# Kernel tuning notes

Measured on AMD Instinct MI355X. Metric: run time of the kernel, lower is better.

Reference implementation:

```python
import jax, jax.numpy as jnp
import numpy as np

B, L, D = 4, 2048, 1024
N_HEADS = 16
D_KV = D // N_HEADS  # 64
TEMPERATURE = D_KV ** 0.5  # 8.0 (note: applied even though heads are never split)


def setup_inputs() -> dict:
    key = jax.random.key(0)
    ks = jax.random.split(key, 7)
    s = 1.0 / np.sqrt(D)
    return {
        "Q": jax.random.normal(ks[0], (B, L, D), jnp.float32),
        "K": jax.random.normal(ks[1], (B, L, D), jnp.float32),
        "V": jax.random.normal(ks[2], (B, L, D), jnp.float32),
        # nn.Linear weights, shape [out, in]; y = x @ W.T
        "W_Q": jax.random.normal(ks[3], (D, D), jnp.float32) * s,
        "W_K": jax.random.normal(ks[4], (D, D), jnp.float32) * s,
        "W_V": jax.random.normal(ks[5], (D, D), jnp.float32) * s,
        "W_O": jax.random.normal(ks[6], (D, D), jnp.float32) * s,
        "masked": 0,
    }


def reference(Q, K, V, W_Q, W_K, W_V, W_O, masked):
    # projections (no bias)
    q = jnp.einsum("bld,ed->ble", Q, W_Q)
    k = jnp.einsum("bld,ed->ble", K, W_K)
    v = jnp.einsum("bld,ed->ble", V, W_V)
    # NOTE: original module never splits heads; scores contract over full d_model
    scores = jnp.einsum("bqe,bke->bqk", q, k) / TEMPERATURE  # [B, L, L]
    if masked:
        # faithful (buggy) original: fill where tril is True
        tril = jnp.tril(jnp.ones((L, L), dtype=bool))
        scores = jnp.where(tril[None], -jnp.inf, scores)
    attn_weights = jax.nn.softmax(scores, axis=-1)
    # dropout(0.1) disabled (eval mode)
    x = jnp.einsum("bqk,bke->bqe", attn_weights, v)
    out = jnp.einsum("ble,de->bld", x, W_O)
    return (out, attn_weights)
```

## Files before the change

### kernel.cpp

```cpp
#include <hip/hip_runtime.h>
#include <math.h>


static constexpr int B_ = 4;
static constexpr int L_ = 2048;
static constexpr int D_ = 1024;

#define BM 128
#define BN 128
#define BKK 64

typedef _Float16 f16x8 __attribute__((ext_vector_type(8)));
typedef float    f32x4 __attribute__((ext_vector_type(4)));
typedef short    s16x8 __attribute__((ext_vector_type(8)));
typedef unsigned short u16x4 __attribute__((ext_vector_type(4)));

typedef __attribute__((address_space(1))) const unsigned int GU32;
typedef __attribute__((address_space(3))) unsigned int LU32;

__device__ __forceinline__ void gload_lds16(const void* g, void* l) {
    __builtin_amdgcn_global_load_lds((GU32*)g, (LU32*)l, 16, 0, 0);
}

__device__ __forceinline__ short f2h_bits(float x) {
    union { _Float16 h; short s; } u;
    u.h = (_Float16)x;
    return u.s;
}

__device__ __forceinline__ s16x8 cvt8h(float4 a, float4 b) {
    union { _Float16 h[8]; s16x8 s; } u;
    u.h[0] = (_Float16)a.x; u.h[1] = (_Float16)a.y;
    u.h[2] = (_Float16)a.z; u.h[3] = (_Float16)a.w;
    u.h[4] = (_Float16)b.x; u.h[5] = (_Float16)b.y;
    u.h[6] = (_Float16)b.z; u.h[7] = (_Float16)b.w;
    return u.s;
}


__device__ __forceinline__ void compute_step(
    const short* __restrict__ As, const short* __restrict__ Bs,
    int wr, int wc, int lr, int lk, f32x4 (&acc)[4][4])
{
#pragma unroll
    for (int kk = 0; kk < 2; ++kk) {
        const int slotk = kk * 4 + lk;
        f16x8 a[4], b[4];
#pragma unroll
        for (int m = 0; m < 4; ++m) {
            const int r = wr * 64 + m * 16 + lr;
            a[m] = *(const f16x8*)&As[r * 64 + ((slotk ^ (r & 7)) << 3)];
        }
#pragma unroll
        for (int n = 0; n < 4; ++n) {
            const int c = wc * 64 + n * 16 + lr;
            b[n] = *(const f16x8*)&Bs[c * 64 + ((slotk ^ (c & 7)) << 3)];
        }
#pragma unroll
        for (int m = 0; m < 4; ++m)
#pragma unroll
            for (int n = 0; n < 4; ++n)
                acc[m][n] = __builtin_amdgcn_mfma_f32_16x16x32_f16(a[m], b[n], acc[m][n], 0, 0, 0);
    }
}

template<int APPLY_SM>
__device__ __forceinline__ void epilogue_f16_bounce(
    short* __restrict__ lw, short* __restrict__ C, long N,
    int bm, int bn, int wr, int wc, int lr, int lk, int lane,
    const f32x4 (&acc)[4][4], float scale, bool msk)
{
#pragma unroll
    for (int m = 0; m < 4; ++m) {
        const int rl0 = m * 16 + lk * 4;
#pragma unroll
        for (int n = 0; n < 4; ++n) {
            const int cl = n * 16 + lr;
            const int slot = cl >> 3, cw = cl & 7;
#pragma unroll
            for (int g = 0; g < 4; ++g) {
                const int rl = rl0 + g;
                float v = acc[m][n][g];
                if constexpr (APPLY_SM) {
                    v *= scale;
                    if (msk && (bn + wc * 64 + cl) <= (bm + wr * 64 + rl)) v = -INFINITY;
                }
                lw[rl * 64 + ((slot ^ (rl & 7)) << 3) + cw] = f2h_bits(v);
            }
        }
    }
    const int l8 = lane & 7, lr8 = lane >> 3;
#pragma unroll
    for (int it = 0; it < 8; ++it) {
        const int rl = it * 8 + lr8;
        const int cl = (l8 ^ (rl & 7)) << 3;
        s16x8 d = *(const s16x8*)&lw[rl * 64 + (l8 << 3)];
        *(s16x8*)&C[(long)(bm + wr * 64 + rl) * N + bn + wc * 64 + cl] = d;
    }
}

template<int OMODE>
__global__ __launch_bounds__(256) void hgemm(
    const short* __restrict__ A16p, const short* __restrict__ Btp, void* __restrict__ Cp_,
    int M, int N, int K, long sA, long sB, long sC,
    float scale, int useMask, const int* __restrict__ mflag)
{
    __shared__ short smem[2 * BM * BKK];
    short* As = smem;
    short* Bs = smem + BM * BKK;

    const int t    = threadIdx.x;
    const int wid  = t >> 6;
    const int lane = t & 63;
    const int bz   = blockIdx.z;

    const int gx = gridDim.x, gy = gridDim.y;
    const int wg = blockIdx.y * gx + blockIdx.x;
    const int bm = (wg % gy) * BM;
    const int bn = (wg / gy) * BN;

    const short* Bt  = Btp + (long)bz * sB;
    const short* A16 = A16p + (long)bz * sA;

    const int wr = wid >> 1, wc = wid & 1;
    const int lr = lane & 15, lk = lane >> 4;
    const int srow = t >> 3, sslot = t & 7;

    f32x4 acc[4][4];
#pragma unroll
    for (int m = 0; m < 4; ++m)
#pragma unroll
        for (int n = 0; n < 4; ++n) acc[m][n] = (f32x4)0.f;

    for (int k0 = 0; k0 < K; k0 += BKK) {
        __syncthreads();
#pragma unroll
        for (int i = 0; i < 4; ++i) {
            const int rb = i * 32 + srow;
            const short* g = Bt + (long)(bn + rb) * K + k0 + ((sslot ^ (rb & 7)) << 3);
            gload_lds16(g, &Bs[i * 2048 + wid * 512]);
        }
#pragma unroll
        for (int i = 0; i < 4; ++i) {
            const int ra = i * 32 + srow;
            const short* g = A16 + (long)(bm + ra) * K + k0 + ((sslot ^ (ra & 7)) << 3);
            gload_lds16(g, &As[i * 2048 + wid * 512]);
        }
        __syncthreads();
        compute_step(As, Bs, wr, wc, lr, lk, acc);
    }

    if constexpr (OMODE == 2) {
        float* C = (float*)Cp_ + (long)bz * sC;
#pragma unroll
        for (int m = 0; m < 4; ++m) {
            const int r0 = bm + wr * 64 + m * 16 + lk * 4;
#pragma unroll
            for (int n = 0; n < 4; ++n) {
                const int c = bn + wc * 64 + n * 16 + lr;
#pragma unroll
                for (int g = 0; g < 4; ++g)
                    C[(long)(r0 + g) * N + c] = acc[m][n][g] * scale;
            }
        }
    } else {
        __syncthreads();
        short* C = (short*)Cp_ + (long)bz * sC;
        epilogue_f16_bounce<0>(smem + wid * 4096, C, N, bm, bn, wr, wc, lr, lk, lane,
                               acc, scale, false);
    }
}


__device__ __forceinline__ void stage8(
    const short* __restrict__ A16, const short* __restrict__ Bt,
    short* __restrict__ As, short* __restrict__ Bs,
    int bm, int bn, int k0, int K, int t, int wid)
{
    const int r0 = t >> 2;
    const int sl = t & 3;
#pragma unroll
    for (int i = 0; i < 2; ++i) {
        const int r = i * 128 + r0;
        const short* g = A16 + (long)(bm + r) * K + k0 + ((sl ^ ((r >> 1) & 3)) << 3);
        gload_lds16(g, As + i * 4096 + wid * 512);
    }
#pragma unroll
    for (int i = 0; i < 2; ++i) {
        const int r = i * 128 + r0;
        const short* g = Bt + (long)(bn + r) * K + k0 + ((sl ^ ((r >> 1) & 3)) << 3);
        gload_lds16(g, Bs + i * 4096 + wid * 512);
    }
}

__device__ __forceinline__ void compute32(
    const short* __restrict__ As, const short* __restrict__ Bs,
    int wr, int wc, int lr, int lk, f32x4 (&acc)[8][4])
{
    f16x8 a[8], b[4];
#pragma unroll
    for (int m = 0; m < 8; ++m) {
        const int r = wr * 128 + m * 16 + lr;
        a[m] = *(const f16x8*)&As[r * 32 + ((lk ^ ((r >> 1) & 3)) << 3)];
    }
#pragma unroll
    for (int n = 0; n < 4; ++n) {
        const int c = wc * 64 + n * 16 + lr;
        b[n] = *(const f16x8*)&Bs[c * 32 + ((lk ^ ((c >> 1) & 3)) << 3)];
    }
    __builtin_amdgcn_s_setprio(1);
#pragma unroll
    for (int m = 0; m < 8; ++m)
#pragma unroll
        for (int n = 0; n < 4; ++n)
            acc[m][n] = __builtin_amdgcn_mfma_f32_16x16x32_f16(a[m], b[n], acc[m][n], 0, 0, 0);
    __builtin_amdgcn_s_setprio(0);
}

template<int APPLY_SM>
__device__ __forceinline__ void epilogue_f16_bounce8(
    short* __restrict__ lw, short* __restrict__ C, long N,
    int rowBase, int colBase, int lr, int lk, int lane,
    const f32x4 (&acc)[8][4], float scale, bool msk)
{
#pragma unroll
    for (int h = 0; h < 2; ++h) {
#pragma unroll
        for (int mm = 0; mm < 4; ++mm) {
            const int m = h * 4 + mm;
            const int rl0 = mm * 16 + lk * 4;
#pragma unroll
            for (int n = 0; n < 4; ++n) {
                const int cl = n * 16 + lr;
                const int slot = cl >> 3, cw = cl & 7;
#pragma unroll
                for (int g = 0; g < 4; ++g) {
                    const int rl = rl0 + g;
                    float v = acc[m][n][g];
                    if constexpr (APPLY_SM) {
                        v *= scale;
                        if (msk && (colBase + cl) <= (rowBase + h * 64 + rl)) v = -INFINITY;
                    }
                    lw[rl * 64 + ((slot ^ (rl & 7)) << 3) + cw] = f2h_bits(v);
                }
            }
        }
        const int l8 = lane & 7, lr8 = lane >> 3;
#pragma unroll
        for (int it = 0; it < 8; ++it) {
            const int rl = it * 8 + lr8;
            const int cl = (l8 ^ (rl & 7)) << 3;
            s16x8 d = *(const s16x8*)&lw[rl * 64 + (l8 << 3)];
            *(s16x8*)&C[(long)(rowBase + h * 64 + rl) * N + colBase + cl] = d;
        }
    }
}

__device__ __forceinline__ void pipeline_loop(
    const short* __restrict__ A16, const short* __restrict__ Bt,
    short* __restrict__ Abuf, short* __restrict__ Bbuf,
    int bm, int bn, int K, int t, int wid,
    int wr, int wc, int lr, int lk, f32x4 (&acc)[8][4])
{
    stage8(A16, Bt, Abuf + 0 * 8192, Bbuf + 0 * 8192, bm, bn, 0,  K, t, wid);
    stage8(A16, Bt, Abuf + 1 * 8192, Bbuf + 1 * 8192, bm, bn, 32, K, t, wid);
    stage8(A16, Bt, Abuf + 2 * 8192, Bbuf + 2 * 8192, bm, bn, 64, K, t, wid);

    const int nt = K / 32;
    for (int ti = 0; ti < nt; ++ti) {
        if (ti + 2 < nt)      asm volatile("s_waitcnt vmcnt(8)" ::: "memory");
        else if (ti + 1 < nt) asm volatile("s_waitcnt vmcnt(4)" ::: "memory");
        else                  asm volatile("s_waitcnt vmcnt(0)" ::: "memory");
        __builtin_amdgcn_sched_barrier(0);
        __builtin_amdgcn_s_barrier();
        __builtin_amdgcn_sched_barrier(0);
        asm volatile("" ::: "memory");
        if (ti + 3 < nt) {
            const int nb = (ti + 3) & 3;
            stage8(A16, Bt, Abuf + nb * 8192, Bbuf + nb * 8192, bm, bn,
                   (ti + 3) * 32, K, t, wid);
        }
        const int cb = ti & 3;
        compute32(Abuf + cb * 8192, Bbuf + cb * 8192, wr, wc, lr, lk, acc);
    }
    __syncthreads();
}

__global__ __launch_bounds__(512) void hgemm8_scores(
    const short* __restrict__ qhp, const short* __restrict__ khp,
    short* __restrict__ Cp, const int* __restrict__ mflag)
{
    __shared__ short smem[65536];

    const int t    = threadIdx.x;
    const int wid  = t >> 6;
    const int lane = t & 63;
    const int bz   = blockIdx.z;
    const int K    = D_;

    const int wg = blockIdx.y * 8 + blockIdx.x;
    const int bm = (wg % 8) * 256;
    const int bn = (wg / 8) * 256;

    const short* A16 = qhp + (long)bz * L_ * D_;
    const short* Bt  = khp + (long)bz * L_ * D_;
    short* C = Cp + (long)bz * ((long)L_ * L_);

    const int wr = wid >> 2, wc = wid & 3;
    const int lr = lane & 15, lk = lane >> 4;

    f32x4 acc[8][4];
#pragma unroll
    for (int m = 0; m < 8; ++m)
#pragma unroll
        for (int n = 0; n < 4; ++n) acc[m][n] = (f32x4)0.f;

    pipeline_loop(A16, Bt, smem, smem + 32768, bm, bn, K, t, wid, wr, wc, lr, lk, acc);

    const bool msk = (mflag[0] != 0);
    epilogue_f16_bounce8<1>(smem + wid * 4096, C, L_,
                            bm + wr * 128, bn + wc * 64, lr, lk, lane,
                            acc, 0.125f, msk);
}

__global__ __launch_bounds__(512) void hgemm8_proj(
    const short* __restrict__ qf, const short* __restrict__ kf, const short* __restrict__ vf,
    const short* __restrict__ wq, const short* __restrict__ wk, const short* __restrict__ wv,
    short* __restrict__ qh, short* __restrict__ kh, short* __restrict__ vT)
{
    __shared__ short smem[65536];

    const int t    = threadIdx.x;
    const int wid  = t >> 6;
    const int lane = t & 63;
    const int bz   = blockIdx.z;
    const int K    = D_;
    const int N    = D_;

    const short* A16 = (bz == 0) ? qf : (bz == 1) ? kf : vf;
    const short* Bt  = (bz == 0) ? wq : (bz == 1) ? wk : wv;

    const int wg = blockIdx.y * 4 + blockIdx.x;
    const int bm = (wg & 31) * 256;
    const int bn = (wg >> 5) * 256;

    const int wr = wid >> 2, wc = wid & 3;
    const int lr = lane & 15, lk = lane >> 4;

    f32x4 acc[8][4];
#pragma unroll
    for (int m = 0; m < 8; ++m)
#pragma unroll
        for (int n = 0; n < 4; ++n) acc[m][n] = (f32x4)0.f;

    pipeline_loop(A16, Bt, smem, smem + 32768, bm, bn, K, t, wid, wr, wc, lr, lk, acc);

    if (bz < 2) {
        short* C = (bz == 0) ? qh : kh;
        epilogue_f16_bounce8<0>(smem + wid * 4096, C, N,
                                bm + wr * 128, bn + wc * 64, lr, lk, lane,
                                acc, 1.f, false);
    } else {
#pragma unroll
        for (int m = 0; m < 8; ++m) {
            const int rg = bm + wr * 128 + m * 16 + lk * 4;
            const long rb = (long)(rg >> 11) * ((long)N * L_) + (rg & (L_ - 1));
#pragma unroll
            for (int n = 0; n < 4; ++n) {
                const int c = bn + wc * 64 + n * 16 + lr;
                u16x4 v;
#pragma unroll
                for (int g = 0; g < 4; ++g) v[g] = (unsigned short)f2h_bits(acc[m][n][g]);
                *(u16x4*)&vT[rb + (long)c * L_] = v;
            }
        }
    }
}


__global__ __launch_bounds__(256) void cvt_w4_k(
    const float* __restrict__ W_Q, const float* __restrict__ W_K,
    const float* __restrict__ W_V, const float* __restrict__ W_O,
    short* __restrict__ dst)
{
    const int w = blockIdx.y;
    const float* src = (w == 0) ? W_Q : (w == 1) ? W_K : (w == 2) ? W_V : W_O;
    short* out = dst + (size_t)w * D_ * D_;
    const int i = blockIdx.x * 256 + threadIdx.x;
    float4 a = ((const float4*)src)[2 * i];
    float4 b = ((const float4*)src)[2 * i + 1];
    *(s16x8*)&out[i * 8] = cvt8h(a, b);
}

__global__ __launch_bounds__(256) void cvt_qkv_k(
    const float* __restrict__ Q, const float* __restrict__ K,
    const float* __restrict__ V, short* __restrict__ dst)
{
    const int w = blockIdx.y;
    const float* src = (w == 0) ? Q : (w == 1) ? K : V;
    short* out = dst + (size_t)w * B_ * L_ * D_;
    const int i = blockIdx.x * 256 + threadIdx.x;
    float4 a = ((const float4*)src)[2 * i];
    float4 b = ((const float4*)src)[2 * i + 1];
    *(s16x8*)&out[i * 8] = cvt8h(a, b);
}

__global__ __launch_bounds__(256) void softmax_rows_k(
    short* __restrict__ S16, float* __restrict__ Sout)
{
    const long row = blockIdx.x;
    short* p16 = S16 + row * (long)L_;
    float* pf  = Sout + row * (long)L_;
    const int tid = threadIdx.x;

    union { s16x8 v; _Float16 h[8]; } u;
    u.v = ((const s16x8*)p16)[tid];
    float f[8];
#pragma unroll
    for (int j = 0; j < 8; ++j) f[j] = (float)u.h[j];

    float m = f[0];
#pragma unroll
    for (int j = 1; j < 8; ++j) m = fmaxf(m, f[j]);
#pragma unroll
    for (int o = 32; o > 0; o >>= 1) m = fmaxf(m, __shfl_xor(m, o, 64));

    __shared__ float wmax[4], wsum[4];
    if ((tid & 63) == 0) wmax[tid >> 6] = m;
    __syncthreads();
    m = fmaxf(fmaxf(wmax[0], wmax[1]), fmaxf(wmax[2], wmax[3]));

    float s = 0.f;
#pragma unroll
    for (int j = 0; j < 8; ++j) { f[j] = expf(f[j] - m); s += f[j]; }
#pragma unroll
    for (int o = 32; o > 0; o >>= 1) s += __shfl_xor(s, o, 64);
    if ((tid & 63) == 0) wsum[tid >> 6] = s;
    __syncthreads();
    s = wsum[0] + wsum[1] + wsum[2] + wsum[3];

    const float inv = 1.f / s;
#pragma unroll
    for (int j = 0; j < 8; ++j) f[j] = f[j] * inv;

    float4 a, b;
    a.x = f[0]; a.y = f[1]; a.z = f[2]; a.w = f[3];
    b.x = f[4]; b.y = f[5]; b.z = f[6]; b.w = f[7];
    ((float4*)pf)[2 * tid]     = a;
    ((float4*)pf)[2 * tid + 1] = b;
    ((s16x8*)p16)[tid] = cvt8h(a, b);
}

extern "C" void kernel_launch(void* const* d_in, const int* in_sizes, int n_in,
                              void* d_out, int out_size, void* d_ws, size_t ws_size,
                              hipStream_t stream) {
    const float* Q   = (const float*)d_in[0];
    const float* K   = (const float*)d_in[1];
    const float* V   = (const float*)d_in[2];
    const float* W_Q = (const float*)d_in[3];
    const float* W_K = (const float*)d_in[4];
    const float* W_V = (const float*)d_in[5];
    const float* W_O = (const float*)d_in[6];
    const int* masked = (const int*)d_in[7];

    float* out  = (float*)d_out;
    float* attn = out + (size_t)B_ * L_ * D_;

    short* wq = (short*)d_ws;
    short* wk = wq + (size_t)D_ * D_;
    short* wv = wk + (size_t)D_ * D_;
    short* wo = wv + (size_t)D_ * D_;
    short* qh = wo + (size_t)D_ * D_;
    short* kh = qh + (size_t)B_ * L_ * D_;
    short* vT = kh + (size_t)B_ * L_ * D_;
    short* attn16 = vT + (size_t)B_ * L_ * D_;
    short* xh = qh;

    short* qf = (short*)attn;
    short* kf = qf + (size_t)B_ * L_ * D_;
    short* vf = kf + (size_t)B_ * L_ * D_;

    const long SLD = (long)L_ * D_;
    const long SLL = (long)L_ * L_;

    cvt_w4_k<<<dim3(D_ * D_ / 8 / 256, 4), 256, 0, stream>>>(W_Q, W_K, W_V, W_O, wq);
    cvt_qkv_k<<<dim3(B_ * L_ * D_ / 8 / 256, 3), 256, 0, stream>>>(Q, K, V, qf);

    hgemm8_proj<<<dim3(4, 32, 3), 512, 0, stream>>>(
        qf, kf, vf, wq, wk, wv, qh, kh, vT);

    hgemm8_scores<<<dim3(8, 8, B_), 512, 0, stream>>>(qh, kh, attn16, masked);

    softmax_rows_k<<<dim3(B_ * L_), 256, 0, stream>>>(attn16, attn);

    dim3 gav(D_ / BN, L_ / BM, B_);
    hgemm<0><<<gav, 256, 0, stream>>>(attn16, vT, xh, L_, D_, L_, SLL, SLD, SLD,
                                      1.f, 0, masked);

    dim3 gproj(D_ / BN, (B_ * L_) / BM, 1);
    hgemm<2><<<gproj, 256, 0, stream>>>(xh, wo, out, B_ * L_, D_, D_, 0, 0, 0,
                                        1.f, 0, masked);
}
```

Measured before the change: 241.6 us.

## Use 4-stage async-pipelined 128x128 GEMM for PV, output and input projections

Replaces the simple double-sync hgemm used for attn@V and the output projection with a new 128x128 tile kernel that uses a 4-deep global-to-LDS prefetch pipeline with vmcnt-based waits and a single barrier per k-step. The QKV projection is also moved from 256x256 tiles with 512 threads to these 128x128 tiles with 256 threads, giving more workgroups. The intent is to hide global load latency and raise occupancy and grid fill. The trade-off is less data reuse per tile in the projection GEMM.

```diff
diff --git a/kernel.cpp b/kernel.cpp
--- a/kernel.cpp
+++ b/kernel.cpp
@@ -5,10 +5,6 @@
 static constexpr int B_ = 4;
 static constexpr int L_ = 2048;
 static constexpr int D_ = 1024;
-
-#define BM 128
-#define BN 128
-#define BKK 64
 
 typedef _Float16 f16x8 __attribute__((ext_vector_type(8)));
 typedef float    f32x4 __attribute__((ext_vector_type(4)));
@@ -38,140 +34,6 @@
 }
 
 
-__device__ __forceinline__ void compute_step(
-    const short* __restrict__ As, const short* __restrict__ Bs,
-    int wr, int wc, int lr, int lk, f32x4 (&acc)[4][4])
-{
-#pragma unroll
-    for (int kk = 0; kk < 2; ++kk) {
-        const int slotk = kk * 4 + lk;
-        f16x8 a[4], b[4];
-#pragma unroll
-        for (int m = 0; m < 4; ++m) {
-            const int r = wr * 64 + m * 16 + lr;
-            a[m] = *(const f16x8*)&As[r * 64 + ((slotk ^ (r & 7)) << 3)];
-        }
-#pragma unroll
-        for (int n = 0; n < 4; ++n) {
-            const int c = wc * 64 + n * 16 + lr;
-            b[n] = *(const f16x8*)&Bs[c * 64 + ((slotk ^ (c & 7)) << 3)];
-        }
-#pragma unroll
-        for (int m = 0; m < 4; ++m)
-#pragma unroll
-            for (int n = 0; n < 4; ++n)
-                acc[m][n] = __builtin_amdgcn_mfma_f32_16x16x32_f16(a[m], b[n], acc[m][n], 0, 0, 0);
-    }
-}
-
-template<int APPLY_SM>
-__device__ __forceinline__ void epilogue_f16_bounce(
-    short* __restrict__ lw, short* __restrict__ C, long N,
-    int bm, int bn, int wr, int wc, int lr, int lk, int lane,
-    const f32x4 (&acc)[4][4], float scale, bool msk)
-{
-#pragma unroll
-    for (int m = 0; m < 4; ++m) {
-        const int rl0 = m * 16 + lk * 4;
-#pragma unroll
-        for (int n = 0; n < 4; ++n) {
-            const int cl = n * 16 + lr;
-            const int slot = cl >> 3, cw = cl & 7;
-#pragma unroll
-            for (int g = 0; g < 4; ++g) {
-                const int rl = rl0 + g;
-                float v = acc[m][n][g];
-                if constexpr (APPLY_SM) {
-                    v *= scale;
-                    if (msk && (bn + wc * 64 + cl) <= (bm + wr * 64 + rl)) v = -INFINITY;
-                }
-                lw[rl * 64 + ((slot ^ (rl & 7)) << 3) + cw] = f2h_bits(v);
-            }
-        }
-    }
-    const int l8 = lane & 7, lr8 = lane >> 3;
-#pragma unroll
-    for (int it = 0; it < 8; ++it) {
-        const int rl = it * 8 + lr8;
-        const int cl = (l8 ^ (rl & 7)) << 3;
-        s16x8 d = *(const s16x8*)&lw[rl * 64 + (l8 << 3)];
-        *(s16x8*)&C[(long)(bm + wr * 64 + rl) * N + bn + wc * 64 + cl] = d;
-    }
-}
-
-template<int OMODE>
-__global__ __launch_bounds__(256) void hgemm(
-    const short* __restrict__ A16p, const short* __restrict__ Btp, void* __restrict__ Cp_,
-    int M, int N, int K, long sA, long sB, long sC,
-    float scale, int useMask, const int* __restrict__ mflag)
-{
-    __shared__ short smem[2 * BM * BKK];
-    short* As = smem;
-    short* Bs = smem + BM * BKK;
-
-    const int t    = threadIdx.x;
-    const int wid  = t >> 6;
-    const int lane = t & 63;
-    const int bz   = blockIdx.z;
-
-    const int gx = gridDim.x, gy = gridDim.y;
-    const int wg = blockIdx.y * gx + blockIdx.x;
-    const int bm = (wg % gy) * BM;
-    const int bn = (wg / gy) * BN;
-
-    const short* Bt  = Btp + (long)bz * sB;
-    const short* A16 = A16p + (long)bz * sA;
-
-    const int wr = wid >> 1, wc = wid & 1;
-    const int lr = lane & 15, lk = lane >> 4;
-    const int srow = t >> 3, sslot = t & 7;
-
-    f32x4 acc[4][4];
-#pragma unroll
-    for (int m = 0; m < 4; ++m)
-#pragma unroll
-        for (int n = 0; n < 4; ++n) acc[m][n] = (f32x4)0.f;
-
-    for (int k0 = 0; k0 < K; k0 += BKK) {
-        __syncthreads();
-#pragma unroll
-        for (int i = 0; i < 4; ++i) {
-            const int rb = i * 32 + srow;
-            const short* g = Bt + (long)(bn + rb) * K + k0 + ((sslot ^ (rb & 7)) << 3);
-            gload_lds16(g, &Bs[i * 2048 + wid * 512]);
-        }
-#pragma unroll
-        for (int i = 0; i < 4; ++i) {
-            const int ra = i * 32 + srow;
-            const short* g = A16 + (long)(bm + ra) * K + k0 + ((sslot ^ (ra & 7)) << 3);
-            gload_lds16(g, &As[i * 2048 + wid * 512]);
-        }
-        __syncthreads();
-        compute_step(As, Bs, wr, wc, lr, lk, acc);
-    }
-
-    if constexpr (OMODE == 2) {
-        float* C = (float*)Cp_ + (long)bz * sC;
-#pragma unroll
-        for (int m = 0; m < 4; ++m) {
-            const int r0 = bm + wr * 64 + m * 16 + lk * 4;
-#pragma unroll
-            for (int n = 0; n < 4; ++n) {
-                const int c = bn + wc * 64 + n * 16 + lr;
-#pragma unroll
-                for (int g = 0; g < 4; ++g)
-                    C[(long)(r0 + g) * N + c] = acc[m][n][g] * scale;
-            }
-        }
-    } else {
-        __syncthreads();
-        short* C = (short*)Cp_ + (long)bz * sC;
-        epilogue_f16_bounce<0>(smem + wid * 4096, C, N, bm, bn, wr, wc, lr, lk, lane,
-                               acc, scale, false);
-    }
-}
-
-
 __device__ __forceinline__ void stage8(
     const short* __restrict__ A16, const short* __restrict__ Bt,
     short* __restrict__ As, short* __restrict__ Bs,
@@ -193,7 +55,7 @@
     }
 }
 
-__device__ __forceinline__ void compute32(
+__device__ __forceinline__ void compute32_w8(
     const short* __restrict__ As, const short* __restrict__ Bs,
     int wr, int wc, int lr, int lk, f32x4 (&acc)[8][4])
 {
@@ -256,7 +118,7 @@
     }
 }
 
-__device__ __forceinline__ void pipeline_loop(
+__device__ __forceinline__ void pipeline_loop8(
     const short* __restrict__ A16, const short* __restrict__ Bt,
     short* __restrict__ Abuf, short* __restrict__ Bbuf,
     int bm, int bn, int K, int t, int wid,
@@ -281,7 +143,7 @@
                    (ti + 3) * 32, K, t, wid);
         }
         const int cb = ti & 3;
-        compute32(Abuf + cb * 8192, Bbuf + cb * 8192, wr, wc, lr, lk, acc);
+        compute32_w8(Abuf + cb * 8192, Bbuf + cb * 8192, wr, wc, lr, lk, acc);
     }
     __syncthreads();
 }
@@ -315,7 +177,7 @@
 #pragma unroll
         for (int n = 0; n < 4; ++n) acc[m][n] = (f32x4)0.f;
 
-    pipeline_loop(A16, Bt, smem, smem + 32768, bm, bn, K, t, wid, wr, wc, lr, lk, acc);
+    pipeline_loop8(A16, Bt, smem, smem + 32768, bm, bn, K, t, wid, wr, wc, lr, lk, acc);
 
     const bool msk = (mflag[0] != 0);
     epilogue_f16_bounce8<1>(smem + wid * 4096, C, L_,
@@ -323,12 +185,168 @@
                             acc, 0.125f, msk);
 }
 
-__global__ __launch_bounds__(512) void hgemm8_proj(
+
+__device__ __forceinline__ void stage4(
+    const short* __restrict__ A16, const short* __restrict__ Bt,
+    short* __restrict__ As, short* __restrict__ Bs,
+    int bm, int bn, int k0, int K, int t, int wid)
+{
+    const int r0 = t >> 2;
+    const int sl = t & 3;
+#pragma unroll
+    for (int i = 0; i < 2; ++i) {
+        const int r = i * 64 + r0;
+        const short* g = A16 + (long)(bm + r) * K + k0 + ((sl ^ ((r >> 1) & 3)) << 3);
+        gload_lds16(g, As + i * 2048 + wid * 512);
+    }
+#pragma unroll
+    for (int i = 0; i < 2; ++i) {
+        const int r = i * 64 + r0;
+        const short* g = Bt + (long)(bn + r) * K + k0 + ((sl ^ ((r >> 1) & 3)) << 3);
+        gload_lds16(g, Bs + i * 2048 + wid * 512);
+    }
+}
+
+__device__ __forceinline__ void compute32_w4(
+    const short* __restrict__ As, const short* __restrict__ Bs,
+    int wr, int wc, int lr, int lk, f32x4 (&acc)[4][4])
+{
+    f16x8 a[4], b[4];
+#pragma unroll
+    for (int m = 0; m < 4; ++m) {
+        const int r = wr * 64 + m * 16 + lr;
+        a[m] = *(const f16x8*)&As[r * 32 + ((lk ^ ((r >> 1) & 3)) << 3)];
+    }
+#pragma unroll
+    for (int n = 0; n < 4; ++n) {
+        const int c = wc * 64 + n * 16 + lr;
+        b[n] = *(const f16x8*)&Bs[c * 32 + ((lk ^ ((c >> 1) & 3)) << 3)];
+    }
+    __builtin_amdgcn_s_setprio(1);
+#pragma unroll
+    for (int m = 0; m < 4; ++m)
+#pragma unroll
+        for (int n = 0; n < 4; ++n)
+            acc[m][n] = __builtin_amdgcn_mfma_f32_16x16x32_f16(a[m], b[n], acc[m][n], 0, 0, 0);
+    __builtin_amdgcn_s_setprio(0);
+}
+
+__device__ __forceinline__ void epilogue_f16_bounce4(
+    short* __restrict__ lw, short* __restrict__ C, long N,
+    int rowBase, int colBase, int lr, int lk, int lane,
+    const f32x4 (&acc)[4][4])
+{
+#pragma unroll
+    for (int m = 0; m < 4; ++m) {
+        const int rl0 = m * 16 + lk * 4;
+#pragma unroll
+        for (int n = 0; n < 4; ++n) {
+            const int cl = n * 16 + lr;
+            const int slot = cl >> 3, cw = cl & 7;
+#pragma unroll
+            for (int g = 0; g < 4; ++g) {
+                const int rl = rl0 + g;
+                lw[rl * 64 + ((slot ^ (rl & 7)) << 3) + cw] = f2h_bits(acc[m][n][g]);
+            }
+        }
+    }
+    const int l8 = lane & 7, lr8 = lane >> 3;
+#pragma unroll
+    for (int it = 0; it < 8; ++it) {
+        const int rl = it * 8 + lr8;
+        const int cl = (l8 ^ (rl & 7)) << 3;
+        s16x8 d = *(const s16x8*)&lw[rl * 64 + (l8 << 3)];
+        *(s16x8*)&C[(long)(rowBase + rl) * N + colBase + cl] = d;
+    }
+}
+
+__device__ __forceinline__ void pipeline_loop4(
+    const short* __restrict__ A16, const short* __restrict__ Bt,
+    short* __restrict__ Abuf, short* __restrict__ Bbuf,
+    int bm, int bn, int K, int t, int wid,
+    int wr, int wc, int lr, int lk, f32x4 (&acc)[4][4])
+{
+    stage4(A16, Bt, Abuf + 0 * 4096, Bbuf + 0 * 4096, bm, bn, 0,  K, t, wid);
+    stage4(A16, Bt, Abuf + 1 * 4096, Bbuf + 1 * 4096, bm, bn, 32, K, t, wid);
+    stage4(A16, Bt, Abuf + 2 * 4096, Bbuf + 2 * 4096, bm, bn, 64, K, t, wid);
+
+    const int nt = K / 32;
+    for (int ti = 0; ti < nt; ++ti) {
+        if (ti + 2 < nt)      asm volatile("s_waitcnt vmcnt(8)" ::: "memory");
+        else if (ti + 1 < nt) asm volatile("s_waitcnt vmcnt(4)" ::: "memory");
+        else                  asm volatile("s_waitcnt vmcnt(0)" ::: "memory");
+        __builtin_amdgcn_sched_barrier(0);
+        __builtin_amdgcn_s_barrier();
+        __builtin_amdgcn_sched_barrier(0);
+        asm volatile("" ::: "memory");
+        if (ti + 3 < nt) {
+            const int nb = (ti + 3) & 3;
+            stage4(A16, Bt, Abuf + nb * 4096, Bbuf + nb * 4096, bm, bn,
+                   (ti + 3) * 32, K, t, wid);
+        }
+        const int cb = ti & 3;
+        compute32_w4(Abuf + cb * 4096, Bbuf + cb * 4096, wr, wc, lr, lk, acc);
+    }
+    __syncthreads();
+}
+
+template<int OMODE>
+__global__ __launch_bounds__(256) void hgemm4_pipe(
+    const short* __restrict__ A16p, const short* __restrict__ Btp, void* __restrict__ Cp_,
+    int N, int K, long sA, long sB, long sC)
+{
+    __shared__ short smem[16384 + 16384];
+
+    const int t    = threadIdx.x;
+    const int wid  = t >> 6;
+    const int lane = t & 63;
+    const int bz   = blockIdx.z;
+
+    const int gx = gridDim.x, gy = gridDim.y;
+    const int wg = blockIdx.y * gx + blockIdx.x;
+    const int bm = (wg % gy) * 128;
+    const int bn = (wg / gy) * 128;
+
+    const short* A16 = A16p + (long)bz * sA;
+    const short* Bt  = Btp + (long)bz * sB;
+
+    const int wr = wid >> 1, wc = wid & 1;
+    const int lr = lane & 15, lk = lane >> 4;
+
+    f32x4 acc[4][4];
+#pragma unroll
+    for (int m = 0; m < 4; ++m)
+#pragma unroll
+        for (int n = 0; n < 4; ++n) acc[m][n] = (f32x4)0.f;
+
+    pipeline_loop4(A16, Bt, smem, smem + 16384, bm, bn, K, t, wid, wr, wc, lr, lk, acc);
+
+    if constexpr (OMODE == 2) {
+        float* C = (float*)Cp_ + (long)bz * sC;
+#pragma unroll
+        for (int m = 0; m < 4; ++m) {
+            const int r0 = bm + wr * 64 + m * 16 + lk * 4;
+#pragma unroll
+            for (int n = 0; n < 4; ++n) {
+                const int c = bn + wc * 64 + n * 16 + lr;
+#pragma unroll
+                for (int g = 0; g < 4; ++g)
+                    C[(long)(r0 + g) * N + c] = acc[m][n][g];
+            }
+        }
+    } else {
+        short* C = (short*)Cp_ + (long)bz * sC;
+        epilogue_f16_bounce4(smem + wid * 4096, C, N,
+                             bm + wr * 64, bn + wc * 64, lr, lk, lane, acc);
+    }
+}
+
+__global__ __launch_bounds__(256) void hgemm4_proj(
     const short* __restrict__ qf, const short* __restrict__ kf, const short* __restrict__ vf,
     const short* __restrict__ wq, const short* __restrict__ wk, const short* __restrict__ wv,
     short* __restrict__ qh, short* __restrict__ kh, short* __restrict__ vT)
 {
-    __shared__ short smem[65536];
+    __shared__ short smem[16384 + 16384];
 
     const int t    = threadIdx.x;
     const int wid  = t >> 6;
@@ -340,30 +358,30 @@
     const short* A16 = (bz == 0) ? qf : (bz == 1) ? kf : vf;
     const short* Bt  = (bz == 0) ? wq : (bz == 1) ? wk : wv;
 
-    const int wg = blockIdx.y * 4 + blockIdx.x;
-    const int bm = (wg & 31) * 256;
-    const int bn = (wg >> 5) * 256;
-
-    const int wr = wid >> 2, wc = wid & 3;
+    const int gx = gridDim.x, gy = gridDim.y;
+    const int wg = blockIdx.y * gx + blockIdx.x;
+    const int bm = (wg % gy) * 128;
+    const int bn = (wg / gy) * 128;
+
+    const int wr = wid >> 1, wc = wid & 1;
     const int lr = lane & 15, lk = lane >> 4;
 
-    f32x4 acc[8][4];
-#pragma unroll
-    for (int m = 0; m < 8; ++m)
+    f32x4 acc[4][4];
+#pragma unroll
+    for (int m = 0; m < 4; ++m)
 #pragma unroll
         for (int n = 0; n < 4; ++n) acc[m][n] = (f32x4)0.f;
 
-    pipeline_loop(A16, Bt, smem, smem + 32768, bm, bn, K, t, wid, wr, wc, lr, lk, acc);
+    pipeline_loop4(A16, Bt, smem, smem + 16384, bm, bn, K, t, wid, wr, wc, lr, lk, acc);
 
     if (bz < 2) {
         short* C = (bz == 0) ? qh : kh;
-        epilogue_f16_bounce8<0>(smem + wid * 4096, C, N,
-                                bm + wr * 128, bn + wc * 64, lr, lk, lane,
-                                acc, 1.f, false);
+        epilogue_f16_bounce4(smem + wid * 4096, C, N,
+                             bm + wr * 64, bn + wc * 64, lr, lk, lane, acc);
     } else {
 #pragma unroll
-        for (int m = 0; m < 8; ++m) {
-            const int rg = bm + wr * 128 + m * 16 + lk * 4;
+        for (int m = 0; m < 4; ++m) {
+            const int rg = bm + wr * 64 + m * 16 + lk * 4;
             const long rb = (long)(rg >> 11) * ((long)N * L_) + (rg & (L_ - 1));
 #pragma unroll
             for (int n = 0; n < 4; ++n) {
@@ -486,18 +504,16 @@
     cvt_w4_k<<<dim3(D_ * D_ / 8 / 256, 4), 256, 0, stream>>>(W_Q, W_K, W_V, W_O, wq);
     cvt_qkv_k<<<dim3(B_ * L_ * D_ / 8 / 256, 3), 256, 0, stream>>>(Q, K, V, qf);
 
-    hgemm8_proj<<<dim3(4, 32, 3), 512, 0, stream>>>(
+    hgemm4_proj<<<dim3(8, 64, 3), 256, 0, stream>>>(
         qf, kf, vf, wq, wk, wv, qh, kh, vT);
 
     hgemm8_scores<<<dim3(8, 8, B_), 512, 0, stream>>>(qh, kh, attn16, masked);
 
     softmax_rows_k<<<dim3(B_ * L_), 256, 0, stream>>>(attn16, attn);
 
-    dim3 gav(D_ / BN, L_ / BM, B_);
-    hgemm<0><<<gav, 256, 0, stream>>>(attn16, vT, xh, L_, D_, L_, SLL, SLD, SLD,
-                                      1.f, 0, masked);
-
-    dim3 gproj(D_ / BN, (B_ * L_) / BM, 1);
-    hgemm<2><<<gproj, 256, 0, stream>>>(xh, wo, out, B_ * L_, D_, D_, 0, 0, 0,
-                                        1.f, 0, masked);
-}
+    hgemm4_pipe<0><<<dim3(8, 16, B_), 256, 0, stream>>>(
+        attn16, vT, xh, D_, L_, SLL, SLD, SLD);
+
+    hgemm4_pipe<2><<<dim3(8, 64, 1), 256, 0, stream>>>(
+        xh, wo, out, D_, D_, 0, 0, 0);
+}
```

Result: faster. 236.9 us (-2.0%).

## Double-buffer 128x128 GEMM loads and use it for projections

Applied to the files above, without the earlier changes.

The 128x128 GEMM gains a two-stage double-buffered pipeline. The next K-tile is issued into the alternate LDS buffer while the current one is computed, and only one barrier is used per iteration. MFMA blocks are wrapped in s_setprio. The QKV projection moves from the 256x256, 512-thread kernel to this 128x128 pipelined kernel with more workgroups, and the unused scale parameters are removed. This trades some per-block reuse and larger tiles for better load/compute overlap and higher occupancy.

```diff
diff --git a/kernel.cpp b/kernel.cpp
--- a/kernel.cpp
+++ b/kernel.cpp
@@ -5,10 +5,6 @@
 static constexpr int B_ = 4;
 static constexpr int L_ = 2048;
 static constexpr int D_ = 1024;
-
-#define BM 128
-#define BN 128
-#define BKK 64
 
 typedef _Float16 f16x8 __attribute__((ext_vector_type(8)));
 typedef float    f32x4 __attribute__((ext_vector_type(4)));
@@ -56,11 +52,32 @@
             const int c = wc * 64 + n * 16 + lr;
             b[n] = *(const f16x8*)&Bs[c * 64 + ((slotk ^ (c & 7)) << 3)];
         }
+        __builtin_amdgcn_s_setprio(1);
 #pragma unroll
         for (int m = 0; m < 4; ++m)
 #pragma unroll
             for (int n = 0; n < 4; ++n)
                 acc[m][n] = __builtin_amdgcn_mfma_f32_16x16x32_f16(a[m], b[n], acc[m][n], 0, 0, 0);
+        __builtin_amdgcn_s_setprio(0);
+    }
+}
+
+__device__ __forceinline__ void stage64(
+    const short* __restrict__ A16, const short* __restrict__ Bt,
+    short* __restrict__ As, short* __restrict__ Bs,
+    int bm, int bn, int k0, int K, int srow, int sslot, int wid)
+{
+#pragma unroll
+    for (int i = 0; i < 4; ++i) {
+        const int rb = i * 32 + srow;
+        const short* g = Bt + (long)(bn + rb) * K + k0 + ((sslot ^ (rb & 7)) << 3);
+        gload_lds16(g, &Bs[i * 2048 + wid * 512]);
+    }
+#pragma unroll
+    for (int i = 0; i < 4; ++i) {
+        const int ra = i * 32 + srow;
+        const short* g = A16 + (long)(bm + ra) * K + k0 + ((sslot ^ (ra & 7)) << 3);
+        gload_lds16(g, &As[i * 2048 + wid * 512]);
     }
 }
 
@@ -99,15 +116,37 @@
     }
 }
 
+__device__ __forceinline__ void pipeline2_64(
+    const short* __restrict__ A16, const short* __restrict__ Bt,
+    short* __restrict__ smem,
+    int bm, int bn, int K, int srow, int sslot, int wid,
+    int wr, int wc, int lr, int lk, f32x4 (&acc)[4][4])
+{
+    stage64(A16, Bt, smem, smem + 8192, bm, bn, 0, K, srow, sslot, wid);
+
+    const int nt = K / 64;
+    for (int ti = 0; ti < nt; ++ti) {
+        asm volatile("s_waitcnt vmcnt(0)" ::: "memory");
+        __builtin_amdgcn_sched_barrier(0);
+        __builtin_amdgcn_s_barrier();
+        __builtin_amdgcn_sched_barrier(0);
+        const int cur = (ti & 1) * 16384;
+        if (ti + 1 < nt) {
+            const int nxt = ((ti + 1) & 1) * 16384;
+            stage64(A16, Bt, smem + nxt, smem + nxt + 8192, bm, bn,
+                    (ti + 1) * 64, K, srow, sslot, wid);
+        }
+        compute_step(smem + cur, smem + cur + 8192, wr, wc, lr, lk, acc);
+    }
+    __syncthreads();
+}
+
 template<int OMODE>
-__global__ __launch_bounds__(256) void hgemm(
+__global__ __launch_bounds__(256) void hgemm64_pipe(
     const short* __restrict__ A16p, const short* __restrict__ Btp, void* __restrict__ Cp_,
-    int M, int N, int K, long sA, long sB, long sC,
-    float scale, int useMask, const int* __restrict__ mflag)
-{
-    __shared__ short smem[2 * BM * BKK];
-    short* As = smem;
-    short* Bs = smem + BM * BKK;
+    int N, int K, long sA, long sB, long sC)
+{
+    __shared__ short smem[32768];
 
     const int t    = threadIdx.x;
     const int wid  = t >> 6;
@@ -116,11 +155,11 @@
 
     const int gx = gridDim.x, gy = gridDim.y;
     const int wg = blockIdx.y * gx + blockIdx.x;
-    const int bm = (wg % gy) * BM;
-    const int bn = (wg / gy) * BN;
-
+    const int bm = (wg % gy) * 128;
+    const int bn = (wg / gy) * 128;
+
+    const short* A16 = A16p + (long)bz * sA;
     const short* Bt  = Btp + (long)bz * sB;
-    const short* A16 = A16p + (long)bz * sA;
 
     const int wr = wid >> 1, wc = wid & 1;
     const int lr = lane & 15, lk = lane >> 4;
@@ -132,23 +171,7 @@
 #pragma unroll
         for (int n = 0; n < 4; ++n) acc[m][n] = (f32x4)0.f;
 
-    for (int k0 = 0; k0 < K; k0 += BKK) {
-        __syncthreads();
-#pragma unroll
-        for (int i = 0; i < 4; ++i) {
-            const int rb = i * 32 + srow;
-            const short* g = Bt + (long)(bn + rb) * K + k0 + ((sslot ^ (rb & 7)) << 3);
-            gload_lds16(g, &Bs[i * 2048 + wid * 512]);
-        }
-#pragma unroll
-        for (int i = 0; i < 4; ++i) {
-            const int ra = i * 32 + srow;
-            const short* g = A16 + (long)(bm + ra) * K + k0 + ((sslot ^ (ra & 7)) << 3);
-            gload_lds16(g, &As[i * 2048 + wid * 512]);
-        }
-        __syncthreads();
-        compute_step(As, Bs, wr, wc, lr, lk, acc);
-    }
+    pipeline2_64(A16, Bt, smem, bm, bn, K, srow, sslot, wid, wr, wc, lr, lk, acc);
 
     if constexpr (OMODE == 2) {
         float* C = (float*)Cp_ + (long)bz * sC;
@@ -160,14 +183,68 @@
                 const int c = bn + wc * 64 + n * 16 + lr;
 #pragma unroll
                 for (int g = 0; g < 4; ++g)
-                    C[(long)(r0 + g) * N + c] = acc[m][n][g] * scale;
+                    C[(long)(r0 + g) * N + c] = acc[m][n][g];
             }
         }
     } else {
-        __syncthreads();
         short* C = (short*)Cp_ + (long)bz * sC;
         epilogue_f16_bounce<0>(smem + wid * 4096, C, N, bm, bn, wr, wc, lr, lk, lane,
-                               acc, scale, false);
+                               acc, 1.f, false);
+    }
+}
+
+__global__ __launch_bounds__(256) void hgemm64_proj(
+    const short* __restrict__ qf, const short* __restrict__ kf, const short* __restrict__ vf,
+    const short* __restrict__ wq, const short* __restrict__ wk, const short* __restrict__ wv,
+    short* __restrict__ qh, short* __restrict__ kh, short* __restrict__ vT)
+{
+    __shared__ short smem[32768];
+
+    const int t    = threadIdx.x;
+    const int wid  = t >> 6;
+    const int lane = t & 63;
+    const int bz   = blockIdx.z;
+    const int K    = D_;
+    const int N    = D_;
+
+    const short* A16 = (bz == 0) ? qf : (bz == 1) ? kf : vf;
+    const short* Bt  = (bz == 0) ? wq : (bz == 1) ? wk : wv;
+
+    const int gx = gridDim.x, gy = gridDim.y;
+    const int wg = blockIdx.y * gx + blockIdx.x;
+    const int bm = (wg % gy) * 128;
+    const int bn = (wg / gy) * 128;
+
+    const int wr = wid >> 1, wc = wid & 1;
+    const int lr = lane & 15, lk = lane >> 4;
+    const int srow = t >> 3, sslot = t & 7;
+
+    f32x4 acc[4][4];
+#pragma unroll
+    for (int m = 0; m < 4; ++m)
+#pragma unroll
+        for (int n = 0; n < 4; ++n) acc[m][n] = (f32x4)0.f;
+
+    pipeline2_64(A16, Bt, smem, bm, bn, K, srow, sslot, wid, wr, wc, lr, lk, acc);
+
+    if (bz < 2) {
+        short* C = (bz == 0) ? qh : kh;
+        epilogue_f16_bounce<0>(smem + wid * 4096, C, N, bm, bn, wr, wc, lr, lk, lane,
+                               acc, 1.f, false);
+    } else {
+#pragma unroll
+        for (int m = 0; m < 4; ++m) {
+            const int rg = bm + wr * 64 + m * 16 + lk * 4;
+            const long rb = (long)(rg >> 11) * ((long)N * L_) + (rg & (L_ - 1));
+#pragma unroll
+            for (int n = 0; n < 4; ++n) {
+                const int c = bn + wc * 64 + n * 16 + lr;
+                u16x4 v;
+#pragma unroll
+                for (int g = 0; g < 4; ++g) v[g] = (unsigned short)f2h_bits(acc[m][n][g]);
+                *(u16x4*)&vT[rb + (long)c * L_] = v;
+            }
+        }
     }
 }
 
@@ -193,7 +270,7 @@
     }
 }
 
-__device__ __forceinline__ void compute32(
+__device__ __forceinline__ void compute32_w8(
     const short* __restrict__ As, const short* __restrict__ Bs,
     int wr, int wc, int lr, int lk, f32x4 (&acc)[8][4])
 {
@@ -256,7 +333,7 @@
     }
 }
 
-__device__ __forceinline__ void pipeline_loop(
+__device__ __forceinline__ void pipeline_loop8(
     const short* __restrict__ A16, const short* __restrict__ Bt,
     short* __restrict__ Abuf, short* __restrict__ Bbuf,
     int bm, int bn, int K, int t, int wid,
@@ -281,7 +358,7 @@
                    (ti + 3) * 32, K, t, wid);
         }
         const int cb = ti & 3;
-        compute32(Abuf + cb * 8192, Bbuf + cb * 8192, wr, wc, lr, lk, acc);
+        compute32_w8(Abuf + cb * 8192, Bbuf + cb * 8192, wr, wc, lr, lk, acc);
     }
     __syncthreads();
 }
@@ -315,66 +392,12 @@
 #pragma unroll
         for (int n = 0; n < 4; ++n) acc[m][n] = (f32x4)0.f;
 
-    pipeline_loop(A16, Bt, smem, smem + 32768, bm, bn, K, t, wid, wr, wc, lr, lk, acc);
+    pipeline_loop8(A16, Bt, smem, smem + 32768, bm, bn, K, t, wid, wr, wc, lr, lk, acc);
 
     const bool msk = (mflag[0] != 0);
     epilogue_f16_bounce8<1>(smem + wid * 4096, C, L_,
                             bm + wr * 128, bn + wc * 64, lr, lk, lane,
                             acc, 0.125f, msk);
-}
-
-__global__ __launch_bounds__(512) void hgemm8_proj(
-    const short* __restrict__ qf, const short* __restrict__ kf, const short* __restrict__ vf,
-    const short* __restrict__ wq, const short* __restrict__ wk, const short* __restrict__ wv,
-    short* __restrict__ qh, short* __restrict__ kh, short* __restrict__ vT)
-{
-    __shared__ short smem[65536];
-
-    const int t    = threadIdx.x;
-    const int wid  = t >> 6;
-    const int lane = t & 63;
-    const int bz   = blockIdx.z;
-    const int K    = D_;
-    const int N    = D_;
-
-    const short* A16 = (bz == 0) ? qf : (bz == 1) ? kf : vf;
-    const short* Bt  = (bz == 0) ? wq : (bz == 1) ? wk : wv;
-
-    const int wg = blockIdx.y * 4 + blockIdx.x;
-    const int bm = (wg & 31) * 256;
-    const int bn = (wg >> 5) * 256;
-
-    const int wr = wid >> 2, wc = wid & 3;
-    const int lr = lane & 15, lk = lane >> 4;
-
-    f32x4 acc[8][4];
-#pragma unroll
-    for (int m = 0; m < 8; ++m)
-#pragma unroll
-        for (int n = 0; n < 4; ++n) acc[m][n] = (f32x4)0.f;
-
-    pipeline_loop(A16, Bt, smem, smem + 32768, bm, bn, K, t, wid, wr, wc, lr, lk, acc);
-
-    if (bz < 2) {
-        short* C = (bz == 0) ? qh : kh;
-        epilogue_f16_bounce8<0>(smem + wid * 4096, C, N,
-                                bm + wr * 128, bn + wc * 64, lr, lk, lane,
-                                acc, 1.f, false);
-    } else {
-#pragma unroll
-        for (int m = 0; m < 8; ++m) {
-            const int rg = bm + wr * 128 + m * 16 + lk * 4;
-            const long rb = (long)(rg >> 11) * ((long)N * L_) + (rg & (L_ - 1));
-#pragma unroll
-            for (int n = 0; n < 4; ++n) {
-                const int c = bn + wc * 64 + n * 16 + lr;
-                u16x4 v;
-#pragma unroll
-                for (int g = 0; g < 4; ++g) v[g] = (unsigned short)f2h_bits(acc[m][n][g]);
-                *(u16x4*)&vT[rb + (long)c * L_] = v;
-            }
-        }
-    }
 }
 
 
@@ -486,18 +509,16 @@
     cvt_w4_k<<<dim3(D_ * D_ / 8 / 256, 4), 256, 0, stream>>>(W_Q, W_K, W_V, W_O, wq);
     cvt_qkv_k<<<dim3(B_ * L_ * D_ / 8 / 256, 3), 256, 0, stream>>>(Q, K, V, qf);
 
-    hgemm8_proj<<<dim3(4, 32, 3), 512, 0, stream>>>(
+    hgemm64_proj<<<dim3(8, 64, 3), 256, 0, stream>>>(
         qf, kf, vf, wq, wk, wv, qh, kh, vT);
 
     hgemm8_scores<<<dim3(8, 8, B_), 512, 0, stream>>>(qh, kh, attn16, masked);
 
     softmax_rows_k<<<dim3(B_ * L_), 256, 0, stream>>>(attn16, attn);
 
-    dim3 gav(D_ / BN, L_ / BM, B_);
-    hgemm<0><<<gav, 256, 0, stream>>>(attn16, vT, xh, L_, D_, L_, SLL, SLD, SLD,
-                                      1.f, 0, masked);
-
-    dim3 gproj(D_ / BN, (B_ * L_) / BM, 1);
-    hgemm<2><<<gproj, 256, 0, stream>>>(xh, wo, out, B_ * L_, D_, D_, 0, 0, 0,
-                                        1.f, 0, masked);
-}
+    hgemm64_pipe<0><<<dim3(8, 16, B_), 256, 0, stream>>>(
+        attn16, vT, xh, D_, L_, SLL, SLD, SLD);
+
+    hgemm64_pipe<2><<<dim3(8, 64, 1), 256, 0, stream>>>(
+        xh, wo, out, D_, D_, 0, 0, 0);
+}
```

Result: faster. 219.0 us (-9.4%).
